# Kernel tuning notes

Hardware: AMD Instinct MI355X
Metric: run time of the kernel (lower is better)

The kernel has to match this reference:

```python
import jax, jax.numpy as jnp
import numpy as np

ATT_NORM = 4.0
EPS = 1e-12

E, H, C, N = 1000000, 8, 16, 100000


def setup_inputs() -> dict:
    key = jax.random.key(0)
    k1, k2, k3, k4, k5 = jax.random.split(key, 5)
    return {
        "x": jax.random.normal(k1, (E, H, C), dtype=jnp.float32),
        "att_l": jax.random.normal(k2, (1, H, C), dtype=jnp.float32),
        "att_r": jax.random.normal(k3, (1, H, C), dtype=jnp.float32),
        "alpha": jax.random.normal(k4, (E, H, 1), dtype=jnp.float32),
        "index": jax.random.randint(k5, (E,), 0, N, dtype=jnp.int32),
        "num_nodes": N,
    }


def reference(x, att_l, att_r, alpha, index, num_nodes):
    # squared L2 norm of per-edge features: [E, H, 1]
    norm_x = jnp.sum(x * x, axis=-1, keepdims=True)
    # scatter-max per destination node: [N, H, 1]
    max_norm_seg = jax.ops.segment_max(norm_x, index, num_segments=num_nodes)
    # gather back per edge and combine: sqrt(max_norm[index] + norm_x)
    max_norm = jnp.sqrt(max_norm_seg[index] + norm_x)  # [E, H, 1]
    # norm of concatenated attention vectors: ||[att_l, att_r]|| over last dim -> [1, H, 1]
    norm_att = ATT_NORM * jnp.sqrt(
        jnp.sum(att_l * att_l, axis=-1, keepdims=True)
        + jnp.sum(att_r * att_r, axis=-1, keepdims=True)
    )
    return alpha / (norm_att * max_norm + EPS)
```

## Files before the change

kernel.cpp:

```cpp
#include <hip/hip_runtime.h>
#include <math.h>

#define EPSF 1e-12f
#define ATT_NORM_F 4.0f
#define H_DIM 8
#define C_DIM 16
#define N_NODES 100000

typedef float v4f __attribute__((ext_vector_type(4)));

__global__ __launch_bounds__(256) void lip_zero(unsigned* __restrict__ p, int n)
{
    int i = blockIdx.x * 256 + threadIdx.x;
    if (i < n) p[i] = 0u;
}

__global__ __launch_bounds__(256) void lip_pass1(
    const float* __restrict__ x, const int* __restrict__ index,
    float* __restrict__ norm_x, unsigned int* __restrict__ seg, int total )
{
    const int stride = gridDim.x * 256;
    const int s0 = blockIdx.x * 256 + threadIdx.x;
    const int lane = s0 & 3;
    const v4f* x4 = (const v4f*)x;

    #pragma unroll 4
    for (int s = s0; s < total; s += stride) {
        v4f v = __builtin_nontemporal_load(&x4[s]);
        float sum = v.x * v.x + v.y * v.y + v.z * v.z + v.w * v.w;
        sum += __shfl_xor(sum, 1);
        sum += __shfl_xor(sum, 2);
        if (lane == 0) {
            int r = s >> 2;
            __builtin_nontemporal_store(sum, &norm_x[r]);
            int e = r >> 3;
            int h = r & 7;
            atomicMax(&seg[(size_t)index[e] * H_DIM + h], __float_as_uint(sum));
        }
    }
}

__global__ __launch_bounds__(256) void lip_pass2(
    const float* __restrict__ norm_x, const float* __restrict__ alpha,
    const int* __restrict__ index, const unsigned int* __restrict__ seg,
    const float* __restrict__ att_l, const float* __restrict__ att_r,
    float* __restrict__ out, int total)
{
    __shared__ float s_natt[H_DIM];
    int t = threadIdx.x;
    if (t < H_DIM) {
        float s = 0.f;
        #pragma unroll
        for (int c = 0; c < C_DIM; ++c) {
            float l = att_l[t * C_DIM + c];
            float r = att_r[t * C_DIM + c];
            s += l * l + r * r;
        }
        s_natt[t] = ATT_NORM_F * sqrtf(s);
    }
    __syncthreads();

    const int stride = gridDim.x * 256;
    const v4f* nx4 = (const v4f*)norm_x;
    const v4f* al4 = (const v4f*)alpha;
    const v4f* sg4 = (const v4f*)seg;
    v4f* out4 = (v4f*)out;

    #pragma unroll 2
    for (int tid = blockIdx.x * 256 + t; tid < total; tid += stride) {
        int e    = tid >> 1;
        int half = tid & 1;
        int idx  = index[e];

        v4f nx = __builtin_nontemporal_load(&nx4[tid]);
        v4f al = __builtin_nontemporal_load(&al4[tid]);
        v4f sg = sg4[(size_t)idx * 2 + half];

        int h0 = half * 4;
        v4f o;
        o.x = al.x / (s_natt[h0 + 0] * sqrtf(sg.x + nx.x) + EPSF);
        o.y = al.y / (s_natt[h0 + 1] * sqrtf(sg.y + nx.y) + EPSF);
        o.z = al.z / (s_natt[h0 + 2] * sqrtf(sg.z + nx.z) + EPSF);
        o.w = al.w / (s_natt[h0 + 3] * sqrtf(sg.w + nx.w) + EPSF);
        __builtin_nontemporal_store(o, &out4[tid]);
    }
}

__global__ __launch_bounds__(256) void lip_pass2_recompute(
    const float* __restrict__ x, const float* __restrict__ alpha,
    const int* __restrict__ index, const unsigned int* __restrict__ seg,
    const float* __restrict__ att_l, const float* __restrict__ att_r,
    float* __restrict__ out, int rows)
{
    __shared__ float s_natt[H_DIM];
    int t = threadIdx.x;
    if (t < H_DIM) {
        float s = 0.f;
        #pragma unroll
        for (int c = 0; c < C_DIM; ++c) {
            float l = att_l[t * C_DIM + c];
            float r = att_r[t * C_DIM + c];
            s += l * l + r * r;
        }
        s_natt[t] = ATT_NORM_F * sqrtf(s);
    }
    __syncthreads();

    int r = blockIdx.x * blockDim.x + t;
    if (r >= rows) return;

    const float4* x4 = (const float4*)x;
    float s = 0.f;
    #pragma unroll
    for (int q = 0; q < 4; ++q) {
        float4 v = x4[(size_t)r * 4 + q];
        s += v.x * v.x + v.y * v.y + v.z * v.z + v.w * v.w;
    }
    int e = r >> 3;
    int h = r & 7;
    float sg = __uint_as_float(seg[(size_t)index[e] * H_DIM + h]);
    out[r] = alpha[r] / (s_natt[h] * sqrtf(sg + s) + EPSF);
}

extern "C" void kernel_launch(void* const* d_in, const int* in_sizes, int n_in,
                              void* d_out, int out_size, void* d_ws, size_t ws_size,
                              hipStream_t stream) {
    const float* x     = (const float*)d_in[0];
    const float* att_l = (const float*)d_in[1];
    const float* att_r = (const float*)d_in[2];
    const float* alpha = (const float*)d_in[3];
    const int*   index = (const int*)d_in[4];

    const int E    = in_sizes[4];
    const int rows = E * H_DIM;

    const int seg_words = N_NODES * H_DIM;
    size_t seg_pad = ((size_t)seg_words * 4 + 255) / 256 * 256;
    size_t need    = seg_pad + (size_t)rows * sizeof(float);

    unsigned* seg = (unsigned*)d_ws;
    lip_zero<<<(seg_words + 255) / 256, 256, 0, stream>>>(seg, seg_words);

    if (ws_size >= need) {
        float* norm_x = (float*)((char*)d_ws + seg_pad);
        lip_pass1<<<2048, 256, 0, stream>>>(x, index, norm_x, seg, rows * 4);
        lip_pass2<<<2048, 256, 0, stream>>>(
            norm_x, alpha, index, seg, att_l, att_r, (float*)d_out, E * 2);
    } else {
        lip_pass1<<<2048, 256, 0, stream>>>(x, index, (float*)d_out, seg, rows * 4);
        lip_pass2_recompute<<<(rows + 255) / 256, 256, 0, stream>>>(
            x, alpha, index, seg, att_l, att_r, (float*)d_out, rows);
    }
}
```

Before: 141.0 us.

## Fuse both passes into one persistent kernel with a grid barrier

Merges the norm/scatter-max pass and the output pass into a single persistent kernel of 1024 blocks. Per-row norms stay in shared memory (31 x 256 floats per block) across a software grid-wide barrier, so the norm_x intermediate never goes to global memory and one launch is dropped. Each thread now reads a full 64-byte row of x itself instead of using a 4-lane shuffle reduction. The risks are that the barrier deadlocks if all 1024 blocks cannot be resident at once, and that about 31 KB of shared memory per block limits occupancy.

Measured after the change: 548.1 us. 3.89x slower.

```diff
diff --git a/kernel.cpp b/kernel.cpp
--- a/kernel.cpp
+++ b/kernel.cpp
@@ -6,6 +6,12 @@
 #define H_DIM 8
 #define C_DIM 16
 #define N_NODES 100000
+#define SEG_WORDS (N_NODES * H_DIM)
+
+#define TPB 256
+#define NBLK 1024
+#define NT (NBLK * TPB)
+#define ITERS 31
 
 typedef float v4f __attribute__((ext_vector_type(4)));
 
@@ -15,26 +21,108 @@
     if (i < n) p[i] = 0u;
 }
 
+__device__ __forceinline__ void grid_barrier(unsigned* bar, unsigned nblk)
+{
+    __syncthreads();
+    if (threadIdx.x == 0) {
+        __threadfence();
+        unsigned g = __hip_atomic_load(&bar[1], __ATOMIC_RELAXED,
+                                       __HIP_MEMORY_SCOPE_AGENT);
+        unsigned old = __hip_atomic_fetch_add(&bar[0], 1u, __ATOMIC_ACQ_REL,
+                                              __HIP_MEMORY_SCOPE_AGENT);
+        if (old == nblk - 1) {
+            __hip_atomic_store(&bar[0], 0u, __ATOMIC_RELAXED,
+                               __HIP_MEMORY_SCOPE_AGENT);
+            __hip_atomic_fetch_add(&bar[1], 1u, __ATOMIC_RELEASE,
+                                   __HIP_MEMORY_SCOPE_AGENT);
+        } else {
+            while (__hip_atomic_load(&bar[1], __ATOMIC_ACQUIRE,
+                                     __HIP_MEMORY_SCOPE_AGENT) == g) {
+                __builtin_amdgcn_s_sleep(2);
+            }
+        }
+        __threadfence();
+    }
+    __syncthreads();
+}
+
+__global__ __launch_bounds__(TPB, 4) void lip_fused(
+    const float* __restrict__ x, const float* __restrict__ att_l,
+    const float* __restrict__ att_r, const float* __restrict__ alpha,
+    const int* __restrict__ index, float* __restrict__ out,
+    unsigned* __restrict__ seg, unsigned* __restrict__ bar, int rows)
+{
+    __shared__ float s_natt[H_DIM];
+    __shared__ float s_nrm[ITERS][TPB];
+
+    const int t = threadIdx.x;
+    if (t < H_DIM) {
+        float s = 0.f;
+        #pragma unroll
+        for (int c = 0; c < C_DIM; ++c) {
+            float l = att_l[t * C_DIM + c];
+            float r = att_r[t * C_DIM + c];
+            s += l * l + r * r;
+        }
+        s_natt[t] = ATT_NORM_F * sqrtf(s);
+    }
+
+    const int tid = blockIdx.x * TPB + t;
+    const v4f* x4 = (const v4f*)x;
+
+    #pragma unroll 2
+    for (int i = 0; i < ITERS; ++i) {
+        int r = tid + i * NT;
+        if (r < rows) {
+            v4f a = __builtin_nontemporal_load(&x4[(size_t)r * 4 + 0]);
+            v4f b = __builtin_nontemporal_load(&x4[(size_t)r * 4 + 1]);
+            v4f c = __builtin_nontemporal_load(&x4[(size_t)r * 4 + 2]);
+            v4f d = __builtin_nontemporal_load(&x4[(size_t)r * 4 + 3]);
+            float s = a.x*a.x + a.y*a.y + a.z*a.z + a.w*a.w
+                    + b.x*b.x + b.y*b.y + b.z*b.z + b.w*b.w
+                    + c.x*c.x + c.y*c.y + c.z*c.z + c.w*c.w
+                    + d.x*d.x + d.y*d.y + d.z*d.z + d.w*d.w;
+            s_nrm[i][t] = s;
+            int e = r >> 3;
+            int h = r & 7;
+            atomicMax(&seg[(size_t)index[e] * H_DIM + h], __float_as_uint(s));
+        }
+    }
+
+    grid_barrier(bar, NBLK);
+
+    #pragma unroll 2
+    for (int i = 0; i < ITERS; ++i) {
+        int r = tid + i * NT;
+        if (r < rows) {
+            int e = r >> 3;
+            int h = r & 7;
+            float sg = __uint_as_float(seg[(size_t)index[e] * H_DIM + h]);
+            float al = __builtin_nontemporal_load(&alpha[r]);
+            float o  = al / (s_natt[h] * sqrtf(sg + s_nrm[i][t]) + EPSF);
+            __builtin_nontemporal_store(o, &out[r]);
+        }
+    }
+}
+
 __global__ __launch_bounds__(256) void lip_pass1(
     const float* __restrict__ x, const int* __restrict__ index,
-    float* __restrict__ norm_x, unsigned int* __restrict__ seg, int total )
+    float* __restrict__ norm_x, unsigned int* __restrict__ seg, int total)
 {
     const int stride = gridDim.x * 256;
     const int s0 = blockIdx.x * 256 + threadIdx.x;
     const int lane = s0 & 3;
     const v4f* x4 = (const v4f*)x;
-
     #pragma unroll 4
     for (int s = s0; s < total; s += stride) {
         v4f v = __builtin_nontemporal_load(&x4[s]);
-        float sum = v.x * v.x + v.y * v.y + v.z * v.z + v.w * v.w;
+        float sum = v.x*v.x + v.y*v.y + v.z*v.z + v.w*v.w;
         sum += __shfl_xor(sum, 1);
         sum += __shfl_xor(sum, 2);
         if (lane == 0) {
             int r = s >> 2;
             __builtin_nontemporal_store(sum, &norm_x[r]);
-            int e = r >> 3;
-            int h = r & 7;
+            int e = r >> 3, h = r & 7;
             atomicMax(&seg[(size_t)index[e] * H_DIM + h], __float_as_uint(sum));
         }
     }
@@ -66,16 +154,14 @@
     const v4f* sg4 = (const v4f*)seg;
     v4f* out4 = (v4f*)out;
 
-    #pragma unroll 2
+    #pragma unroll 4
     for (int tid = blockIdx.x * 256 + t; tid < total; tid += stride) {
-        int e    = tid >> 1;
+        int e = tid >> 1;
         int half = tid & 1;
-        int idx  = index[e];
-
-        v4f nx = __builtin_nontemporal_load(&nx4[tid]);
+        int idx = index[e];
+        v4f nx = nx4[tid];
         v4f al = __builtin_nontemporal_load(&al4[tid]);
         v4f sg = sg4[(size_t)idx * 2 + half];
-
         int h0 = half * 4;
         v4f o;
         o.x = al.x / (s_natt[h0 + 0] * sqrtf(sg.x + nx.x) + EPSF);
@@ -84,42 +170,6 @@
         o.w = al.w / (s_natt[h0 + 3] * sqrtf(sg.w + nx.w) + EPSF);
         __builtin_nontemporal_store(o, &out4[tid]);
     }
-}
-
-__global__ __launch_bounds__(256) void lip_pass2_recompute(
-    const float* __restrict__ x, const float* __restrict__ alpha,
-    const int* __restrict__ index, const unsigned int* __restrict__ seg,
-    const float* __restrict__ att_l, const float* __restrict__ att_r,
-    float* __restrict__ out, int rows)
-{
-    __shared__ float s_natt[H_DIM];
-    int t = threadIdx.x;
-    if (t < H_DIM) {
-        float s = 0.f;
-        #pragma unroll
-        for (int c = 0; c < C_DIM; ++c) {
-            float l = att_l[t * C_DIM + c];
-            float r = att_r[t * C_DIM + c];
-            s += l * l + r * r;
-        }
-        s_natt[t] = ATT_NORM_F * sqrtf(s);
-    }
-    __syncthreads();
-
-    int r = blockIdx.x * blockDim.x + t;
-    if (r >= rows) return;
-
-    const float4* x4 = (const float4*)x;
-    float s = 0.f;
-    #pragma unroll
-    for (int q = 0; q < 4; ++q) {
-        float4 v = x4[(size_t)r * 4 + q];
-        s += v.x * v.x + v.y * v.y + v.z * v.z + v.w * v.w;
-    }
-    int e = r >> 3;
-    int h = r & 7;
-    float sg = __uint_as_float(seg[(size_t)index[e] * H_DIM + h]);
-    out[r] = alpha[r] / (s_natt[h] * sqrtf(sg + s) + EPSF);
 }
 
 extern "C" void kernel_launch(void* const* d_in, const int* in_sizes, int n_in,
@@ -134,21 +184,23 @@
     const int E    = in_sizes[4];
     const int rows = E * H_DIM;
 
-    const int seg_words = N_NODES * H_DIM;
-    size_t seg_pad = ((size_t)seg_words * 4 + 255) / 256 * 256;
-    size_t need    = seg_pad + (size_t)rows * sizeof(float);
+    const int zero_words = SEG_WORDS + 2;
+    size_t seg_pad = ((size_t)zero_words * 4 + 255) / 256 * 256;
+    size_t need_fb = seg_pad + (size_t)rows * 4;
 
     unsigned* seg = (unsigned*)d_ws;
-    lip_zero<<<(seg_words + 255) / 256, 256, 0, stream>>>(seg, seg_words);
-
-    if (ws_size >= need) {
+    unsigned* bar = seg + SEG_WORDS;
+
+    if (rows <= ITERS * NT && ws_size >= (size_t)zero_words * 4) {
+        lip_zero<<<(zero_words + 255) / 256, 256, 0, stream>>>(seg, zero_words);
+        lip_fused<<<NBLK, TPB, 0, stream>>>(
+            x, att_l, att_r, alpha, index, (float*)d_out, seg, bar, rows);
+    } else {
         float* norm_x = (float*)((char*)d_ws + seg_pad);
+        lip_zero<<<(SEG_WORDS + 255) / 256, 256, 0, stream>>>(seg, SEG_WORDS);
         lip_pass1<<<2048, 256, 0, stream>>>(x, index, norm_x, seg, rows * 4);
         lip_pass2<<<2048, 256, 0, stream>>>(
             norm_x, alpha, index, seg, att_l, att_r, (float*)d_out, E * 2);
-    } else {
-        lip_pass1<<<2048, 256, 0, stream>>>(x, index, (float*)d_out, seg, rows * 4);
-        lip_pass2_recompute<<<(rows + 255) / 256, 256, 0, stream>>>(
-            x, alpha, index, seg, att_l, att_r, (float*)d_out, rows);
-    }
-}
+        (void)need_fb;
+    }
+}
```
